# Performance work log

Measured on AMD Instinct MI355X. Metric: run time of the kernel, lower is better.

The kernel has to match this reference:

```python
import jax, jax.numpy as jnp
import numpy as np

HID = 2048
HEADS = 16
HD = HID // HEADS  # 128
EPS = 1e-6


def setup_inputs() -> dict:
    key = jax.random.key(0)
    ks = jax.random.split(key, 9)
    s = 1.0 / np.sqrt(HID)
    return {
        "hidden_states": jax.random.normal(ks[0], (4, 4096, HID), jnp.float32),
        "q_w": jax.random.normal(ks[1], (HID, HID), jnp.float32) * s,
        "q_b": jnp.zeros((HID,), jnp.float32),
        "k_w": jax.random.normal(ks[2], (HID, HID), jnp.float32) * s,
        "k_b": jnp.zeros((HID,), jnp.float32),
        "v_w": jax.random.normal(ks[3], (HID, HID), jnp.float32) * s,
        "v_b": jnp.zeros((HID,), jnp.float32),
        "o_w": jax.random.normal(ks[4], (HID, HID), jnp.float32) * s,
        "o_b": jnp.zeros((HID,), jnp.float32),
    }


def _heads(x, b, s):
    # [B,S,HID] -> [B,H,S,Dh]
    return x.reshape(b, s, HEADS, HD).transpose(0, 2, 1, 3)


def reference(hidden_states, q_w, q_b, k_w, k_b, v_w, v_b, o_w, o_b):
    b, s, _ = hidden_states.shape
    # torch Linear: y = x @ W.T + b
    q = _heads(hidden_states @ q_w.T + q_b, b, s)
    k = _heads(hidden_states @ k_w.T + k_b, b, s)
    v = _heads(hidden_states @ v_w.T + v_b, b, s)
    # kernel feature map: elu(x) + 1
    qp = jax.nn.elu(q) + 1.0
    kp = jax.nn.elu(k) + 1.0
    # KV outer-product reduction over sequence: [B,H,Dh,Dh]
    kv = jnp.einsum('bhsd,bhse->bhde', kp, v)
    # normalizer z = q' @ sum_s k'  -> [B,H,S,1]
    z = jnp.einsum('bhsd,bhd->bhs', qp, kp.sum(axis=2))[..., None]
    attn = jnp.einsum('bhsd,bhde->bhse', qp, kv) / (z + EPS)
    out = attn.transpose(0, 2, 1, 3).reshape(b, s, HID)
    return out @ o_w.T + o_b
```

## Files before the change

### kernel.cpp

```cpp
#include <hip/hip_runtime.h>
#include <hip/hip_bf16.h>

#define HIDC 2048
#define NHEADS 16
#define HDIM 128
#define NB 4
#define NS 4096
#define NROWS (NB*NS)
#define QSTR 6144
#define EPSV 1e-6f

typedef __attribute__((ext_vector_type(8))) short s16x8;
typedef __attribute__((ext_vector_type(4))) float f32x4;
typedef __attribute__((ext_vector_type(16))) float f32x16;
typedef __attribute__((ext_vector_type(8))) unsigned short u16x8;

static __device__ __forceinline__ unsigned short f2b(float f) {
  unsigned int u = __float_as_uint(f);
  u += 0x7fffu + ((u >> 16) & 1u);
  return (unsigned short)(u >> 16);
}
static __device__ __forceinline__ float b2f(unsigned short h) {
  return __uint_as_float(((unsigned int)h) << 16);
}

static __device__ __forceinline__ void gload_lds16(const unsigned short* g, unsigned short* l) {
  __builtin_amdgcn_global_load_lds(
      (const __attribute__((address_space(1))) void*)g,
      (__attribute__((address_space(3))) void*)l, 16, 0, 0);
}

__global__ __launch_bounds__(256) void convert_all(
    const float* __restrict__ hs, const float* __restrict__ qw,
    const float* __restrict__ kw, const float* __restrict__ vw,
    const float* __restrict__ ow,
    unsigned short* __restrict__ hsb, unsigned short* __restrict__ qwb,
    unsigned short* __restrict__ kwb, unsigned short* __restrict__ vwb,
    unsigned short* __restrict__ owb)
{
  int bid = blockIdx.x;
  const float* src; unsigned short* dst; size_t base;
  if (bid < 16384) { src = hs; dst = hsb; base = (size_t)bid << 11; }
  else {
    int t = bid - 16384; int wsel = t >> 11; int wb = t & 2047;
    src = wsel == 0 ? qw : wsel == 1 ? kw : wsel == 2 ? vw : ow;
    dst = wsel == 0 ? qwb : wsel == 1 ? kwb : wsel == 2 ? vwb : owb;
    base = (size_t)wb << 11;
  }
  size_t i = base + ((size_t)threadIdx.x << 3);
  float4 a = *(const float4*)(src + i);
  float4 b = *(const float4*)(src + i + 4);
  u16x8 o;
  o[0] = f2b(a.x); o[1] = f2b(a.y); o[2] = f2b(a.z); o[3] = f2b(a.w);
  o[4] = f2b(b.x); o[5] = f2b(b.y); o[6] = f2b(b.z); o[7] = f2b(b.w);
  *(u16x8*)(dst + i) = o;
}

template<int QKV, int OUT_BF16>
__global__ __launch_bounds__(512, 1) void gemm256(
    const unsigned short* __restrict__ A,
    const unsigned short* __restrict__ B0,
    const unsigned short* __restrict__ B1,
    const unsigned short* __restrict__ B2,
    const float* __restrict__ bias0,
    const float* __restrict__ bias1,
    const float* __restrict__ bias2,
    void* __restrict__ Cp,
    int ntile, int astr, int ostr)
{
  __shared__ unsigned short lds[65536];
  const int tid = threadIdx.x;
  const int lane = tid & 63, wid = tid >> 6;
  const int wr = wid >> 2, wc = wid & 3;
  const int l31 = lane & 31, l5 = lane >> 5;

  const int cpx = (int)gridDim.x >> 3;
  const int bidx = (int)blockIdx.x;
  const int wg = (bidx & 7) * cpx + (bidx >> 3);
  const int csz = ntile << 2;
  const int chunk = wg / csz;
  const int tt = wg % csz;
  const int bm = ((chunk << 2) + (tt & 3)) << 8;
  const int bn = (tt >> 2) << 8;

  const unsigned short* Bp = B0;
  const float* bias = bias0;
  bool act = false;
  int bnw = bn;
  if (QKV) {
    int seg = bn >> 11;
    Bp = seg == 0 ? B0 : (seg == 1 ? B1 : B2);
    bias = seg == 0 ? bias0 : (seg == 1 ? bias1 : bias2);
    act = seg < 2;
    bnw = bn & 2047;
  }

  const int r0 = tid >> 2;
  const int s0 = tid & 3;
  const int scol = ((s0 ^ ((r0 >> 3) & 3)) << 3);
  const unsigned short* ApA  = A  + (size_t)(bm  + r0) * astr + scol;
  const unsigned short* ApA2 = ApA + (size_t)128 * astr;
  const unsigned short* BpB  = Bp + (size_t)(bnw + r0) * HIDC + scol;
  const unsigned short* BpB2 = BpB + (size_t)128 * HIDC;

  const int xr = (l31 >> 3) & 3;
  const int sj0 = ((l5 ^ xr) << 3);
  const int sj1 = (((2 + l5) ^ xr) << 3);
  const int abase = ((wr << 7) + l31) * 32;
  const int bbase = 16384 + ((wc << 6) + l31) * 32;

  f32x16 acc[4][2] = {};
  s16x8 a[4][2], b[2][2];

#define LD(off_) (*(const s16x8*)&lds[off_])
#define ST_A(kk_, kt_) { \
    gload_lds16(ApA  + (kt_) + ((kk_) << 5), &lds[wb + ((kk_) << 13) + (tid << 3)]); \
    gload_lds16(ApA2 + (kt_) + ((kk_) << 5), &lds[wb + ((kk_) << 13) + 4096 + (tid << 3)]); }
#define ST_B(kk_, kt_) { \
    gload_lds16(BpB  + (kt_) + ((kk_) << 5), &lds[wb + 16384 + ((kk_) << 13) + (tid << 3)]); \
    gload_lds16(BpB2 + (kt_) + ((kk_) << 5), &lds[wb + 16384 + ((kk_) << 13) + 4096 + (tid << 3)]); }
#define MM8(j_) { \
    acc[0][0] = __builtin_amdgcn_mfma_f32_32x32x16_bf16(a[0][j_], b[0][j_], acc[0][0], 0, 0, 0); \
    acc[0][1] = __builtin_amdgcn_mfma_f32_32x32x16_bf16(a[0][j_], b[1][j_], acc[0][1], 0, 0, 0); \
    acc[1][0] = __builtin_amdgcn_mfma_f32_32x32x16_bf16(a[1][j_], b[0][j_], acc[1][0], 0, 0, 0); \
    acc[1][1] = __builtin_amdgcn_mfma_f32_32x32x16_bf16(a[1][j_], b[1][j_], acc[1][1], 0, 0, 0); \
    acc[2][0] = __builtin_amdgcn_mfma_f32_32x32x16_bf16(a[2][j_], b[0][j_], acc[2][0], 0, 0, 0); \
    acc[2][1] = __builtin_amdgcn_mfma_f32_32x32x16_bf16(a[2][j_], b[1][j_], acc[2][1], 0, 0, 0); \
    acc[3][0] = __builtin_amdgcn_mfma_f32_32x32x16_bf16(a[3][j_], b[0][j_], acc[3][0], 0, 0, 0); \
    acc[3][1] = __builtin_amdgcn_mfma_f32_32x32x16_bf16(a[3][j_], b[1][j_], acc[3][1], 0, 0, 0); }
#define SB   __builtin_amdgcn_sched_barrier(0);
#define BAR  __builtin_amdgcn_s_barrier();
#define PRON __builtin_amdgcn_s_setprio(1);
#define PROFF __builtin_amdgcn_s_setprio(0);

#define PHASE(rb_, kk_, GATE, STG, kts_) { \
    if ((GATE) == 4)      { asm volatile("s_waitcnt vmcnt(4)" ::: "memory"); } \
    else if ((GATE) == 0) { asm volatile("s_waitcnt vmcnt(0)" ::: "memory"); } \
    BAR \
    const int pb = (rb_) + ((kk_) << 13); \
    b[0][0] = LD(pb + bbase + sj0); \
    b[1][0] = LD(pb + bbase + 1024 + sj0); \
    a[0][0] = LD(pb + abase + sj0); \
    a[1][0] = LD(pb + abase + 1024 + sj0); \
    a[2][0] = LD(pb + abase + 2048 + sj0); \
    a[3][0] = LD(pb + abase + 3072 + sj0); \
    if (STG) { ST_A(kk_, kts_); ST_B(kk_, kts_); } \
    b[0][1] = LD(pb + bbase + sj1); \
    b[1][1] = LD(pb + bbase + 1024 + sj1); \
    a[0][1] = LD(pb + abase + sj1); \
    a[1][1] = LD(pb + abase + 1024 + sj1); \
    a[2][1] = LD(pb + abase + 2048 + sj1); \
    a[3][1] = LD(pb + abase + 3072 + sj1); \
    SB PRON MM8(0) MM8(1) PROFF \
  }

  {
    const int wb = 0;
    ST_A(0, 0); ST_B(0, 0);
    ST_A(1, 0); ST_B(1, 0);
  }

  for (int t = 0; t < 31; ++t) {
    const int rb = (t & 1) << 15;
    const int wb = rb ^ 32768;
    const int kts = (t + 1) << 6;
    PHASE(rb, 0, 4, 1, kts)
    PHASE(rb, 1, 4, 1, kts)
  }
  {
    const int rb = (31 & 1) << 15;
    const int wb = 0; (void)wb;
    PHASE(rb, 0, 4, 0, 0)
    PHASE(rb, 1, 0, 0, 0)
  }

#undef PHASE
#undef PROFF
#undef PRON
#undef BAR
#undef SB
#undef MM8
#undef ST_B
#undef ST_A
#undef LD

  #pragma unroll
  for (int mf = 0; mf < 4; ++mf) {
    #pragma unroll
    for (int nf = 0; nf < 2; ++nf) {
      const int colw = (wc << 6) + (nf << 5) + l31;
      const float bv = bias[bnw + colw];
      #pragma unroll
      for (int reg = 0; reg < 16; ++reg) {
        const int row = bm + (wr << 7) + (mf << 5) + (reg & 3) + ((reg >> 2) << 3) + (l5 << 2);
        float v = acc[mf][nf][reg] + bv;
        if (QKV) { if (act) v = (v > 0.f) ? (v + 1.f) : __expf(v); }
        const size_t off = (size_t)row * ostr + bn + colw;
        if (OUT_BF16) ((unsigned short*)Cp)[off] = f2b(v);
        else          ((float*)Cp)[off] = v;
      }
    }
  }
}

__global__ __launch_bounds__(256) void kv_partial(
    const unsigned short* __restrict__ kp, const unsigned short* __restrict__ vv,
    float* __restrict__ kvp, float* __restrict__ ksp)
{
  const int bh = blockIdx.x >> 4;
  const int chunk = blockIdx.x & 15;
  const int b = bh >> 4, h = bh & 15;
  const int tid = threadIdx.x;
  const int td = tid >> 4, te = tid & 15;

  __shared__ float kpl[32][128];
  __shared__ float vl[32][132];

  float acc[8][8] = {};
  float ks[8] = {};

  const size_t rowbase = (size_t)b * NS * QSTR + (size_t)h * HDIM;
  const int s0 = chunk * 256;

  for (int st = 0; st < 256; st += 32) {
    __syncthreads();
    #pragma unroll
    for (int i = 0; i < 2; ++i) {
      int idx = tid + (i << 8);
      int row = idx >> 4, q = idx & 15;
      size_t g = rowbase + (size_t)(s0 + st + row) * QSTR + (q << 3);
      u16x8 k8 = *(const u16x8*)(kp + g);
      u16x8 v8 = *(const u16x8*)(vv + g);
      float tk[8], tv[8];
      #pragma unroll
      for (int j = 0; j < 8; ++j) { tk[j] = b2f(k8[j]); tv[j] = b2f(v8[j]); }
      *(float4*)&kpl[row][(q << 3)]     = make_float4(tk[0], tk[1], tk[2], tk[3]);
      *(float4*)&kpl[row][(q << 3) + 4] = make_float4(tk[4], tk[5], tk[6], tk[7]);
      *(float4*)&vl[row][(q << 3)]      = make_float4(tv[0], tv[1], tv[2], tv[3]);
      *(float4*)&vl[row][(q << 3) + 4]  = make_float4(tv[4], tv[5], tv[6], tv[7]);
    }
    __syncthreads();
    #pragma unroll 4
    for (int s = 0; s < 32; ++s) {
      float kd[8], ve[8];
      *(float4*)&kd[0] = *(const float4*)&kpl[s][td << 3];
      *(float4*)&kd[4] = *(const float4*)&kpl[s][(td << 3) + 4];
      *(float4*)&ve[0] = *(const float4*)&vl[s][te << 3];
      *(float4*)&ve[4] = *(const float4*)&vl[s][(te << 3) + 4];
      if (te == 0) {
        #pragma unroll
        for (int i = 0; i < 8; ++i) ks[i] += kd[i];
      }
      #pragma unroll
      for (int i = 0; i < 8; ++i)
        #pragma unroll
        for (int j = 0; j < 8; ++j)
          acc[i][j] += kd[i] * ve[j];
    }
  }

  float* outp = kvp + ((size_t)(chunk * 64 + bh) << 14);
  #pragma unroll
  for (int j = 0; j < 8; ++j) {
    int e = (te << 3) + j;
    float r0[8];
    #pragma unroll
    for (int i = 0; i < 8; ++i) r0[i] = acc[i][j];
    *(float4*)&outp[(size_t)e * HDIM + (td << 3)]     = *(float4*)&r0[0];
    *(float4*)&outp[(size_t)e * HDIM + (td << 3) + 4] = *(float4*)&r0[4];
  }
  if (te == 0) {
    float* kso = ksp + ((size_t)(chunk * 64 + bh) << 7) + (td << 3);
    #pragma unroll
    for (int i = 0; i < 8; ++i) kso[i] = ks[i];
  }
}

__global__ __launch_bounds__(256) void kv_reduce(
    const float* __restrict__ kvp, unsigned short* __restrict__ kvTb,
    const float* __restrict__ ksp, float* __restrict__ ksumf)
{
  int i = blockIdx.x * 256 + threadIdx.x;
  float s = 0.f;
  #pragma unroll
  for (int c = 0; c < 16; ++c) s += kvp[(size_t)c * (64 * 16384) + i];
  kvTb[i] = f2b(s);
  if (blockIdx.x < 32) {
    int j = blockIdx.x * 256 + threadIdx.x;
    float t = 0.f;
    #pragma unroll
    for (int c = 0; c < 16; ++c) t += ksp[c * 8192 + j];
    ksumf[j] = t;
  }
}

__global__ __launch_bounds__(256) void attn2(
    const unsigned short* __restrict__ qp, const unsigned short* __restrict__ kvTb,
    const float* __restrict__ ksumf, unsigned short* __restrict__ attn)
{
  const int bh = blockIdx.x >> 5, stile = blockIdx.x & 31;
  const int b = bh >> 4, h = bh & 15;
  const int tid = threadIdx.x;
  const int lane = tid & 63, wid = tid >> 6;
  const int wr = wid >> 1, wc = wid & 1;
  const int l31 = lane & 31, l5 = lane >> 5;

  __shared__ unsigned short qs[16384];
  __shared__ float ksl[128];
  __shared__ float zsh[256];
  __shared__ float zs[128];

  const size_t qbase = ((size_t)b * NS + (size_t)stile * 128) * QSTR + (size_t)h * HDIM;

  #pragma unroll
  for (int i = 0; i < 8; ++i) {
    int idx = tid + (i << 8);
    int r = idx >> 4, s = idx & 15;
    gload_lds16(qp + qbase + (size_t)r * QSTR + ((s ^ (r & 15)) << 3), &qs[idx << 3]);
  }
  if (tid < 32) {
    *(float4*)&ksl[tid << 2] = *(const float4*)(ksumf + (bh << 7) + (tid << 2));
  }
  __syncthreads();

  {
    const int row = tid >> 1, half = tid & 1;
    const unsigned short* qr = qp + qbase + (size_t)row * QSTR + (half << 6);
    float zp = 0.f;
    #pragma unroll
    for (int q8 = 0; q8 < 8; ++q8) {
      u16x8 v8 = *(const u16x8*)(qr + (q8 << 3));
      #pragma unroll
      for (int j = 0; j < 8; ++j) zp += b2f(v8[j]) * ksl[(half << 6) + (q8 << 3) + j];
    }
    zsh[tid] = zp;
  }
  __syncthreads();
  if ((tid & 1) == 0) {
    const int row = tid >> 1;
    zs[row] = 1.f / (zsh[tid] + zsh[tid + 1] + EPSV);
  }
  __syncthreads();

  f32x16 acc[2][2] = {};
  const unsigned short* kvb = kvTb + ((size_t)bh << 14);
  const unsigned short* bp0 = kvb + (((wc << 6) + l31) << 7) + (l5 << 3);
  const int ar0 = (wr << 6) + l31;
  const int ar1 = ar0 + 32;
  #pragma unroll
  for (int kk = 0; kk < 8; ++kk) {
    const int sN = (kk << 1) + l5;
    s16x8 a0 = *(const s16x8*)&qs[(ar0 << 7) + ((sN ^ (ar0 & 15)) << 3)];
    s16x8 a1 = *(const s16x8*)&qs[(ar1 << 7) + ((sN ^ (ar1 & 15)) << 3)];
    s16x8 b0 = *(const s16x8*)(bp0 + (kk << 4));
    s16x8 b1 = *(const s16x8*)(bp0 + 4096 + (kk << 4));
    acc[0][0] = __builtin_amdgcn_mfma_f32_32x32x16_bf16(a0, b0, acc[0][0], 0, 0, 0);
    acc[0][1] = __builtin_amdgcn_mfma_f32_32x32x16_bf16(a0, b1, acc[0][1], 0, 0, 0);
    acc[1][0] = __builtin_amdgcn_mfma_f32_32x32x16_bf16(a1, b0, acc[1][0], 0, 0, 0);
    acc[1][1] = __builtin_amdgcn_mfma_f32_32x32x16_bf16(a1, b1, acc[1][1], 0, 0, 0);
  }

  #pragma unroll
  for (int mf = 0; mf < 2; ++mf) {
    #pragma unroll
    for (int nf = 0; nf < 2; ++nf) {
      const int e = (wc << 6) + (nf << 5) + l31;
      #pragma unroll
      for (int reg = 0; reg < 16; ++reg) {
        const int row = (wr << 6) + (mf << 5) + (reg & 3) + ((reg >> 2) << 3) + (l5 << 2);
        attn[qbase + (size_t)row * QSTR + e] = f2b(acc[mf][nf][reg] * zs[row]);
      }
    }
  }
}

extern "C" void kernel_launch(void* const* d_in, const int* in_sizes, int n_in,
                              void* d_out, int out_size, void* d_ws, size_t ws_size,
                              hipStream_t stream) {
  const float* hs = (const float*)d_in[0];
  const float* qw = (const float*)d_in[1];
  const float* qb = (const float*)d_in[2];
  const float* kw = (const float*)d_in[3];
  const float* kb = (const float*)d_in[4];
  const float* vw = (const float*)d_in[5];
  const float* vb = (const float*)d_in[6];
  const float* ow = (const float*)d_in[7];
  const float* ob = (const float*)d_in[8];

  char* w = (char*)d_ws;
  unsigned short* hsb = (unsigned short*)(w);
  unsigned short* qwb = (unsigned short*)(w + 67108864);
  unsigned short* kwb = (unsigned short*)(w + 75497472);
  unsigned short* vwb = (unsigned short*)(w + 83886080);
  unsigned short* owb = (unsigned short*)(w + 92274688);
  unsigned short* qkv = (unsigned short*)(w + 100663296);
  float* kvp = (float*)(w);
  float* ksp = (float*)(w + 67108864);
  unsigned short* kvTb = (unsigned short*)(w + 67108864 + 524288);
  float* ksumf = (float*)(w + 67108864 + 524288 + 2097152);

  convert_all<<<dim3(24576), dim3(256), 0, stream>>>(hs, qw, kw, vw, ow, hsb, qwb, kwb, vwb, owb);
  gemm256<1, 1><<<dim3(1536), dim3(512), 0, stream>>>(
      hsb, qwb, kwb, vwb, qb, kb, vb, qkv, 24, HIDC, QSTR);
  kv_partial<<<dim3(1024), dim3(256), 0, stream>>>(qkv + 2048, qkv + 4096, kvp, ksp);
  kv_reduce<<<dim3(4096), dim3(256), 0, stream>>>(kvp, kvTb, ksp, ksumf);
  attn2<<<dim3(2048), dim3(256), 0, stream>>>(qkv, kvTb, ksumf, qkv + 4096);
  gemm256<0, 0><<<dim3(512), dim3(512), 0, stream>>>(
      qkv + 4096, owb, owb, owb, ob, ob, ob, d_out, 8, QSTR, HIDC);
}
```

Measured before the change: 771.9 us.

## Restructure GEMM main loop into 4-stage LDS ring with register double-buffering

Replaces the two-buffer, two-phase-per-iteration K loop with a four-slot LDS ring of 32-wide K stages, issuing global loads three stages ahead. LDS fragments for the next stage are read into a second register set while the MFMAs for the current stage run, with lgkmcnt waits placed so LDS reads overlap matrix math. The aim is to hide LDS read latency and cut barrier stalls before each MFMA block. In exchange the fragment registers double, which raises VGPR pressure and may lower occupancy, and the hand-written waitcnt and barrier ordering is easy to get subtly wrong.

```diff
diff --git a/kernel.cpp b/kernel.cpp
--- a/kernel.cpp
+++ b/kernel.cpp
@@ -107,81 +107,77 @@
   const int sj0 = ((l5 ^ xr) << 3);
   const int sj1 = (((2 + l5) ^ xr) << 3);
   const int abase = ((wr << 7) + l31) * 32;
-  const int bbase = 16384 + ((wc << 6) + l31) * 32;
+  const int bbase = 8192 + ((wc << 6) + l31) * 32;
 
   f32x16 acc[4][2] = {};
-  s16x8 a[4][2], b[2][2];
+  s16x8 ar[2][4][2], br[2][2][2];
 
 #define LD(off_) (*(const s16x8*)&lds[off_])
-#define ST_A(kk_, kt_) { \
-    gload_lds16(ApA  + (kt_) + ((kk_) << 5), &lds[wb + ((kk_) << 13) + (tid << 3)]); \
-    gload_lds16(ApA2 + (kt_) + ((kk_) << 5), &lds[wb + ((kk_) << 13) + 4096 + (tid << 3)]); }
-#define ST_B(kk_, kt_) { \
-    gload_lds16(BpB  + (kt_) + ((kk_) << 5), &lds[wb + 16384 + ((kk_) << 13) + (tid << 3)]); \
-    gload_lds16(BpB2 + (kt_) + ((kk_) << 5), &lds[wb + 16384 + ((kk_) << 13) + 4096 + (tid << 3)]); }
-#define MM8(j_) { \
-    acc[0][0] = __builtin_amdgcn_mfma_f32_32x32x16_bf16(a[0][j_], b[0][j_], acc[0][0], 0, 0, 0); \
-    acc[0][1] = __builtin_amdgcn_mfma_f32_32x32x16_bf16(a[0][j_], b[1][j_], acc[0][1], 0, 0, 0); \
-    acc[1][0] = __builtin_amdgcn_mfma_f32_32x32x16_bf16(a[1][j_], b[0][j_], acc[1][0], 0, 0, 0); \
-    acc[1][1] = __builtin_amdgcn_mfma_f32_32x32x16_bf16(a[1][j_], b[1][j_], acc[1][1], 0, 0, 0); \
-    acc[2][0] = __builtin_amdgcn_mfma_f32_32x32x16_bf16(a[2][j_], b[0][j_], acc[2][0], 0, 0, 0); \
-    acc[2][1] = __builtin_amdgcn_mfma_f32_32x32x16_bf16(a[2][j_], b[1][j_], acc[2][1], 0, 0, 0); \
-    acc[3][0] = __builtin_amdgcn_mfma_f32_32x32x16_bf16(a[3][j_], b[0][j_], acc[3][0], 0, 0, 0); \
-    acc[3][1] = __builtin_amdgcn_mfma_f32_32x32x16_bf16(a[3][j_], b[1][j_], acc[3][1], 0, 0, 0); }
+#define ST4(s_) { const int wb = ((s_) & 3) << 14; const int kt = (s_) << 5; \
+    gload_lds16(ApA  + kt, &lds[wb + (tid << 3)]); \
+    gload_lds16(ApA2 + kt, &lds[wb + 4096 + (tid << 3)]); \
+    gload_lds16(BpB  + kt, &lds[wb + 8192 + (tid << 3)]); \
+    gload_lds16(BpB2 + kt, &lds[wb + 12288 + (tid << 3)]); }
+#define RD12(s_, Q_) { const int rb = ((s_) & 3) << 14; \
+    br[Q_][0][0] = LD(rb + bbase + sj0);        br[Q_][0][1] = LD(rb + bbase + sj1); \
+    br[Q_][1][0] = LD(rb + bbase + 1024 + sj0); br[Q_][1][1] = LD(rb + bbase + 1024 + sj1); \
+    ar[Q_][0][0] = LD(rb + abase + sj0);        ar[Q_][0][1] = LD(rb + abase + sj1); \
+    ar[Q_][1][0] = LD(rb + abase + 1024 + sj0); ar[Q_][1][1] = LD(rb + abase + 1024 + sj1); \
+    ar[Q_][2][0] = LD(rb + abase + 2048 + sj0); ar[Q_][2][1] = LD(rb + abase + 2048 + sj1); \
+    ar[Q_][3][0] = LD(rb + abase + 3072 + sj0); ar[Q_][3][1] = LD(rb + abase + 3072 + sj1); }
+#define MM16(P_) { \
+    acc[0][0] = __builtin_amdgcn_mfma_f32_32x32x16_bf16(ar[P_][0][0], br[P_][0][0], acc[0][0], 0, 0, 0); \
+    acc[0][1] = __builtin_amdgcn_mfma_f32_32x32x16_bf16(ar[P_][0][0], br[P_][1][0], acc[0][1], 0, 0, 0); \
+    acc[1][0] = __builtin_amdgcn_mfma_f32_32x32x16_bf16(ar[P_][1][0], br[P_][0][0], acc[1][0], 0, 0, 0); \
+    acc[1][1] = __builtin_amdgcn_mfma_f32_32x32x16_bf16(ar[P_][1][0], br[P_][1][0], acc[1][1], 0, 0, 0); \
+    acc[2][0] = __builtin_amdgcn_mfma_f32_32x32x16_bf16(ar[P_][2][0], br[P_][0][0], acc[2][0], 0, 0, 0); \
+    acc[2][1] = __builtin_amdgcn_mfma_f32_32x32x16_bf16(ar[P_][2][0], br[P_][1][0], acc[2][1], 0, 0, 0); \
+    acc[3][0] = __builtin_amdgcn_mfma_f32_32x32x16_bf16(ar[P_][3][0], br[P_][0][0], acc[3][0], 0, 0, 0); \
+    acc[3][1] = __builtin_amdgcn_mfma_f32_32x32x16_bf16(ar[P_][3][0], br[P_][1][0], acc[3][1], 0, 0, 0); \
+    acc[0][0] = __builtin_amdgcn_mfma_f32_32x32x16_bf16(ar[P_][0][1], br[P_][0][1], acc[0][0], 0, 0, 0); \
+    acc[0][1] = __builtin_amdgcn_mfma_f32_32x32x16_bf16(ar[P_][0][1], br[P_][1][1], acc[0][1], 0, 0, 0); \
+    acc[1][0] = __builtin_amdgcn_mfma_f32_32x32x16_bf16(ar[P_][1][1], br[P_][0][1], acc[1][0], 0, 0, 0); \
+    acc[1][1] = __builtin_amdgcn_mfma_f32_32x32x16_bf16(ar[P_][1][1], br[P_][1][1], acc[1][1], 0, 0, 0); \
+    acc[2][0] = __builtin_amdgcn_mfma_f32_32x32x16_bf16(ar[P_][2][1], br[P_][0][1], acc[2][0], 0, 0, 0); \
+    acc[2][1] = __builtin_amdgcn_mfma_f32_32x32x16_bf16(ar[P_][2][1], br[P_][1][1], acc[2][1], 0, 0, 0); \
+    acc[3][0] = __builtin_amdgcn_mfma_f32_32x32x16_bf16(ar[P_][3][1], br[P_][0][1], acc[3][0], 0, 0, 0); \
+    acc[3][1] = __builtin_amdgcn_mfma_f32_32x32x16_bf16(ar[P_][3][1], br[P_][1][1], acc[3][1], 0, 0, 0); }
 #define SB   __builtin_amdgcn_sched_barrier(0);
-#define BAR  __builtin_amdgcn_s_barrier();
 #define PRON __builtin_amdgcn_s_setprio(1);
 #define PROFF __builtin_amdgcn_s_setprio(0);
 
-#define PHASE(rb_, kk_, GATE, STG, kts_) { \
-    if ((GATE) == 4)      { asm volatile("s_waitcnt vmcnt(4)" ::: "memory"); } \
-    else if ((GATE) == 0) { asm volatile("s_waitcnt vmcnt(0)" ::: "memory"); } \
-    BAR \
-    const int pb = (rb_) + ((kk_) << 13); \
-    b[0][0] = LD(pb + bbase + sj0); \
-    b[1][0] = LD(pb + bbase + 1024 + sj0); \
-    a[0][0] = LD(pb + abase + sj0); \
-    a[1][0] = LD(pb + abase + 1024 + sj0); \
-    a[2][0] = LD(pb + abase + 2048 + sj0); \
-    a[3][0] = LD(pb + abase + 3072 + sj0); \
-    if (STG) { ST_A(kk_, kts_); ST_B(kk_, kts_); } \
-    b[0][1] = LD(pb + bbase + sj1); \
-    b[1][1] = LD(pb + bbase + 1024 + sj1); \
-    a[0][1] = LD(pb + abase + sj1); \
-    a[1][1] = LD(pb + abase + 1024 + sj1); \
-    a[2][1] = LD(pb + abase + 2048 + sj1); \
-    a[3][1] = LD(pb + abase + 3072 + sj1); \
-    SB PRON MM8(0) MM8(1) PROFF \
-  }
-
-  {
-    const int wb = 0;
-    ST_A(0, 0); ST_B(0, 0);
-    ST_A(1, 0); ST_B(1, 0);
-  }
-
-  for (int t = 0; t < 31; ++t) {
-    const int rb = (t & 1) << 15;
-    const int wb = rb ^ 32768;
-    const int kts = (t + 1) << 6;
-    PHASE(rb, 0, 4, 1, kts)
-    PHASE(rb, 1, 4, 1, kts)
-  }
-  {
-    const int rb = (31 & 1) << 15;
-    const int wb = 0; (void)wb;
-    PHASE(rb, 0, 4, 0, 0)
-    PHASE(rb, 1, 0, 0, 0)
-  }
-
-#undef PHASE
+#define STEP(s_, P_, RD_, STG_, GATE_, BAR_) { \
+    if (RD_) RD12((s_) + 1, 1 - (P_)); \
+    if (STG_) ST4((s_) + 3); \
+    if (RD_) { asm volatile("s_waitcnt lgkmcnt(12)" ::: "memory"); } \
+    else     { asm volatile("s_waitcnt lgkmcnt(0)"  ::: "memory"); } \
+    SB PRON MM16(P_) PROFF \
+    if ((GATE_) == 4)      { asm volatile("s_waitcnt vmcnt(4)" ::: "memory"); } \
+    else if ((GATE_) == 0) { asm volatile("s_waitcnt vmcnt(0)" ::: "memory"); } \
+    if (BAR_) __builtin_amdgcn_s_barrier(); \
+  }
+
+  ST4(0); ST4(1); ST4(2);
+  asm volatile("s_waitcnt vmcnt(4)" ::: "memory");
+  __builtin_amdgcn_s_barrier();
+  RD12(0, 0);
+
+  for (int s = 0; s < 60; s += 2) {
+    STEP(s,     0, 1, 1, 4, 1)
+    STEP(s + 1, 1, 1, 1, 4, 1)
+  }
+  STEP(60, 0, 1, 1, 4, 1)
+  STEP(61, 1, 1, 0, 0, 1)
+  STEP(62, 0, 1, 0, -1, 0)
+  STEP(63, 1, 0, 0, -1, 0)
+
+#undef STEP
 #undef PROFF
 #undef PRON
-#undef BAR
 #undef SB
-#undef MM8
-#undef ST_B
-#undef ST_A
+#undef MM16
+#undef RD12
+#undef ST4
 #undef LD
 
   #pragma unroll
```

After: 795.6 us. 1.03x slower.
